# Optimization experiments

Measured on AMD Instinct MI355X. Metric: run time of the kernel, lower is better.

Reference implementation:

```python
import jax, jax.numpy as jnp
import numpy as np

B, S, E, C = 128, 512, 768, 9


def setup_inputs() -> dict:
    key = jax.random.key(0)
    ks = jax.random.split(key, 7)
    return {
        "enc": jax.random.normal(ks[0], (B, S, E), dtype=jnp.float32),
        "W": jax.random.normal(ks[1], (C, E), dtype=jnp.float32) * 0.02,
        "b": jax.random.normal(ks[2], (C,), dtype=jnp.float32) * 0.02,
        "start_transitions": jax.random.normal(ks[3], (C,), dtype=jnp.float32) * 0.1,
        "end_transitions": jax.random.normal(ks[4], (C,), dtype=jnp.float32) * 0.1,
        "transitions": jax.random.normal(ks[5], (C, C), dtype=jnp.float32) * 0.1,
        "tags": jax.random.randint(ks[6], (B, S), 0, C, dtype=jnp.int64),
        "mask": jnp.ones((B, S), dtype=bool),
    }


def _crf_nll_mean(emissions, tags, mask, start_transitions, end_transitions, transitions):
    # emissions: [B,S,C], tags: [B,S] int, mask: [B,S] bool (mask[:,0] all True)
    maskf = mask.astype(emissions.dtype)
    b_idx = jnp.arange(emissions.shape[0])
    # ---- numerator: score of the gold tag path ----
    em_tag = jnp.take_along_axis(emissions, tags[..., None], axis=2)[..., 0]  # [B,S]
    trans_pair = transitions[tags[:, :-1], tags[:, 1:]]  # [B,S-1]
    num = start_transitions[tags[:, 0]] + em_tag[:, 0]
    num = num + jnp.sum((trans_pair + em_tag[:, 1:]) * maskf[:, 1:], axis=1)
    seq_len = mask.sum(axis=1).astype(jnp.int32)
    last_tags = tags[b_idx, seq_len - 1]
    num = num + end_transitions[last_tags]
    # ---- denominator: forward algorithm (log partition) via scan ----
    def step(alpha, xs):
        em_t, m_t = xs  # [B,C], [B]
        # broadcast: alpha[b,i] + transitions[i,j] + em_t[b,j]
        nxt = jax.nn.logsumexp(alpha[:, :, None] + transitions[None, :, :] + em_t[:, None, :], axis=1)
        alpha = jnp.where(m_t[:, None], nxt, alpha)
        return alpha, None

    alpha0 = start_transitions[None, :] + emissions[:, 0]  # [B,C]
    em_rest = jnp.swapaxes(emissions[:, 1:], 0, 1)  # [S-1,B,C]
    m_rest = jnp.swapaxes(mask[:, 1:], 0, 1)        # [S-1,B]
    alpha, _ = jax.lax.scan(step, alpha0, (em_rest, m_rest))
    den = jax.nn.logsumexp(alpha + end_transitions[None, :], axis=1)  # [B]
    # reduction='mean' over batch; module returns -llh
    return jnp.mean(den - num)


def reference(enc, W, b, start_transitions, end_transitions, transitions, tags, mask):
    # BERT output `enc` is frozen (torch.no_grad); dropout omitted (deterministic ref)
    emissions = jnp.einsum("bse,ce->bsc", enc, W) + b  # linear head [B,S,C]
    return _crf_nll_mean(emissions, tags, mask, start_transitions, end_transitions, transitions)
```

## Files before the change

### kernel.cpp

```cpp
#include <hip/hip_runtime.h>

static constexpr int kB = 128;
static constexpr int kS = 512;
static constexpr int kE = 768;
static constexpr int kC = 9;
static constexpr int kT = 16;
static constexpr int kChunks = 32;

using bf16x8 = __attribute__((ext_vector_type(8))) short;
using f32x4  = __attribute__((ext_vector_type(4))) float;

__device__ __forceinline__ unsigned short f2bf(float f) {
  union { float f; unsigned u; } cv; cv.f = f;
  return (unsigned short)((cv.u + 0x7FFFu + ((cv.u >> 16) & 1u)) >> 16);
}

__global__ __launch_bounds__(256) void wconv_kernel(const float* __restrict__ W,
                                                    unsigned short* __restrict__ Wbf) {
  const int idx = blockIdx.x * 256 + threadIdx.x;
  if (idx < 16 * kE) Wbf[idx] = (idx < kC * kE) ? f2bf(W[idx]) : (unsigned short)0;
}

__global__ __launch_bounds__(128) void fused_chunk(
    const float* __restrict__ enc, const unsigned short* __restrict__ Wbf,
    const float* __restrict__ bias, const float* __restrict__ trans,
    const float* __restrict__ start_t, const float* __restrict__ end_t,
    const int* __restrict__ tags, float* __restrict__ Pout,
    float* __restrict__ numP) {
  __shared__ float emt[2 * kT * 12];
  __shared__ float P[81];
  __shared__ float atmp[16];
  __shared__ float nred[kT];

  const int blk = blockIdx.x;
  const int b = blk >> 5;
  const int k = blk & 31;
  const int tid = threadIdx.x;
  const int wv = tid >> 6;
  const int lane = tid & 63;
  const int mn = lane & 15;
  const int quad = lane >> 4;

  {
    const float* rp = enc + ((size_t)(b * kS + k * kT + mn)) * kE + wv * (kE / 2) + quad * 8;
    const unsigned short* wp = Wbf + mn * kE + wv * (kE / 2) + quad * 8;
    f32x4 acc = {0.f, 0.f, 0.f, 0.f};
#pragma unroll 4
    for (int s = 0; s < (kE / 2) / 32; ++s) {
      const float4 x0 = *reinterpret_cast<const float4*>(rp + s * 32);
      const float4 x1 = *reinterpret_cast<const float4*>(rp + s * 32 + 4);
      bf16x8 a;
      a[0] = (short)f2bf(x0.x); a[1] = (short)f2bf(x0.y);
      a[2] = (short)f2bf(x0.z); a[3] = (short)f2bf(x0.w);
      a[4] = (short)f2bf(x1.x); a[5] = (short)f2bf(x1.y);
      a[6] = (short)f2bf(x1.z); a[7] = (short)f2bf(x1.w);
      const bf16x8 bf = *reinterpret_cast<const bf16x8*>(wp + s * 32);
      acc = __builtin_amdgcn_mfma_f32_16x16x32_bf16(a, bf, acc, 0, 0, 0);
    }
    if (mn < kC) {
      const float bc = (wv == 0) ? bias[mn] : 0.f;
#pragma unroll
      for (int r = 0; r < 4; ++r)
        emt[wv * (kT * 12) + (quad * 4 + r) * 12 + mn] = acc[r] + bc;
    }
  }
  __syncthreads();

#define EM(t, c) (emt[(t) * 12 + (c)] + emt[kT * 12 + (t) * 12 + (c)])

  if (tid < kT) {
    const int t = k * kT + tid;
    const int ct = tags[b * kS + t];
    float v = EM(tid, ct);
    if (t == 0) v += start_t[ct];
    else        v += trans[tags[b * kS + t - 1] * kC + ct];
    if (t == kS - 1) v += end_t[ct];
    nred[tid] = v;
  }
  __syncthreads();
  if (tid == 0) {
    float s = 0.f;
#pragma unroll
    for (int i = 0; i < kT; ++i) s += nred[i];
    numP[blk] = s;
  }

  const bool act = tid < 81;
  const int ci = act ? (tid / 9) : 0;
  const int cj = act ? (tid - ci * 9) : 0;
  float tr[kC];
  if (act) {
#pragma unroll
    for (int kk = 0; kk < kC; ++kk) tr[kk] = trans[kk * kC + cj];
  }

  if (k == 0) {
    if (tid < kC) atmp[tid] = start_t[tid] + EM(0, tid);
    __syncthreads();
    for (int t = 1; t < kT; ++t) {
      float nv = 0.f;
      if (tid < kC) {
        float m = -3.0e38f, v[kC];
#pragma unroll
        for (int i = 0; i < kC; ++i) { v[i] = atmp[i] + tr[i]; m = fmaxf(m, v[i]); }
        float s = 0.f;
#pragma unroll
        for (int i = 0; i < kC; ++i) s += __expf(v[i] - m);
        nv = m + __logf(s) + EM(t, tid);
      }
      __syncthreads();
      if (tid < kC) atmp[tid] = nv;
      __syncthreads();
    }
    if (tid < kC) Pout[(size_t)blk * 81 + tid] = atmp[tid];
  } else {
    if (act) P[tid] = trans[ci * kC + cj] + EM(0, cj);
    __syncthreads();
    for (int t = 1; t < kT; ++t) {
      float nv = 0.f;
      if (act) {
        float m = -3.0e38f, v[kC];
#pragma unroll
        for (int kk = 0; kk < kC; ++kk) { v[kk] = P[ci * 9 + kk] + tr[kk]; m = fmaxf(m, v[kk]); }
        float s = 0.f;
#pragma unroll
        for (int kk = 0; kk < kC; ++kk) s += __expf(v[kk] - m);
        nv = m + __logf(s) + EM(t, cj);
      }
      __syncthreads();
      if (act) P[tid] = nv;
      __syncthreads();
    }
    if (act) Pout[(size_t)blk * 81 + cj * kC + ci] = P[tid];
  }
#undef EM
}

__global__ __launch_bounds__(64) void combine_kernel(const float* __restrict__ Pmat,
                                                     const float* __restrict__ numP,
                                                     const float* __restrict__ end_t,
                                                     float* __restrict__ out) {
  const int b = blockIdx.x;
  const int lane = threadIdx.x;

  float nsum = (lane < kChunks) ? numP[b * kChunks + lane] : 0.f;
#pragma unroll
  for (int m = 16; m >= 1; m >>= 1) nsum += __shfl_down(nsum, m, 64);

  const float* Pb = Pmat + (size_t)b * kChunks * 81;
  const int ln = (lane < kC) ? lane : 0;
  float alpha = Pb[ln];

  float p[kC];
#pragma unroll
  for (int i = 0; i < kC; ++i) p[i] = Pb[81 + ln * kC + i];

  for (int k = 1; k < kChunks; ++k) {
    float pn[kC];
    if (k + 1 < kChunks) {
      const float* Pn = Pb + (k + 1) * 81 + ln * kC;
#pragma unroll
      for (int i = 0; i < kC; ++i) pn[i] = Pn[i];
    }
    float tv[kC];
    float m = -3.0e38f;
#pragma unroll
    for (int i = 0; i < kC; ++i) {
      const float ai = __shfl(alpha, i, 64);
      tv[i] = ai + p[i];
      m = fmaxf(m, tv[i]);
    }
    float s = 0.f;
#pragma unroll
    for (int i = 0; i < kC; ++i) s += __expf(tv[i] - m);
    alpha = m + __logf(s);
#pragma unroll
    for (int i = 0; i < kC; ++i) p[i] = pn[i];
  }

  const float v = alpha + end_t[ln];
  float vv[kC];
  float m = -3.0e38f;
#pragma unroll
  for (int i = 0; i < kC; ++i) {
    vv[i] = __shfl(v, i, 64);
    m = fmaxf(m, vv[i]);
  }
  float s = 0.f;
#pragma unroll
  for (int i = 0; i < kC; ++i) s += __expf(vv[i] - m);
  if (lane == 0) {
    const float den = m + __logf(s);
    atomicAdd(out, (den - nsum) * (1.0f / (float)kB));
  }
}

extern "C" void kernel_launch(void* const* d_in, const int* in_sizes, int n_in,
                              void* d_out, int out_size, void* d_ws, size_t ws_size,
                              hipStream_t stream) {
  const float* enc   = (const float*)d_in[0];
  const float* W     = (const float*)d_in[1];
  const float* bias  = (const float*)d_in[2];
  const float* start = (const float*)d_in[3];
  const float* end_t = (const float*)d_in[4];
  const float* trans = (const float*)d_in[5];
  const int*   tags  = (const int*)d_in[6];

  unsigned short* Wbf = (unsigned short*)d_ws;
  float* Pmat = (float*)((char*)d_ws + 16 * kE * sizeof(unsigned short));
  float* numP = Pmat + (size_t)kB * kChunks * 81;
  float* out  = (float*)d_out;

  hipMemsetAsync(out, 0, sizeof(float), stream);
  hipLaunchKernelGGL(wconv_kernel, dim3((16 * kE + 255) / 256), dim3(256), 0, stream, W, Wbf);
  hipLaunchKernelGGL(fused_chunk, dim3(kB * kChunks), dim3(128), 0, stream,
                     enc, Wbf, bias, trans, start, end_t, tags, Pmat, numP);
  hipLaunchKernelGGL(combine_kernel, dim3(kB), dim3(64), 0, stream, Pmat, numP, end_t, out);
}
```

Baseline: 308.0 us.

## Run chunk scan in one wavefront with wave barriers and packed bf16 conversion

The per-chunk forward scan is moved from a two-wave block using __syncthreads to a single wavefront. Each lane handles up to two of the 81 matrix entries, with wave barriers and float4 LDS reads. The second wave now only computes the gold-path numerator with shuffles and exits early. The emission partial sums are merged into one LDS buffer, and fp32→bf16 conversion uses the packed HIP intrinsic. The aim is to cut block-wide barrier cost and conversion instructions, at the cost of a more serial per-lane workload in the scan.

```diff
diff --git a/kernel.cpp b/kernel.cpp
--- a/kernel.cpp
+++ b/kernel.cpp
@@ -1,4 +1,5 @@
 #include <hip/hip_runtime.h>
+#include <hip/hip_bf16.h>
 
 static constexpr int kB = 128;
 static constexpr int kS = 512;
@@ -15,6 +16,13 @@
   return (unsigned short)((cv.u + 0x7FFFu + ((cv.u >> 16) & 1u)) >> 16);
 }
 
+__device__ __forceinline__ short2 cvt2(float lo, float hi) {
+  const __hip_bfloat162 h = __float22bfloat162_rn(make_float2(lo, hi));
+  short2 r;
+  __builtin_memcpy(&r, &h, sizeof(r));
+  return r;
+}
+
 __global__ __launch_bounds__(256) void wconv_kernel(const float* __restrict__ W,
                                                     unsigned short* __restrict__ Wbf) {
   const int idx = blockIdx.x * 256 + threadIdx.x;
@@ -27,10 +35,8 @@
     const float* __restrict__ start_t, const float* __restrict__ end_t,
     const int* __restrict__ tags, float* __restrict__ Pout,
     float* __restrict__ numP) {
-  __shared__ float emt[2 * kT * 12];
-  __shared__ float P[81];
-  __shared__ float atmp[16];
-  __shared__ float nred[kT];
+  __shared__ __align__(16) float emt[kT * 12];
+  __shared__ __align__(16) float P[kC * 12];
 
   const int blk = blockIdx.x;
   const int b = blk >> 5;
@@ -41,99 +47,129 @@
   const int mn = lane & 15;
   const int quad = lane >> 4;
 
+  f32x4 acc = {0.f, 0.f, 0.f, 0.f};
   {
     const float* rp = enc + ((size_t)(b * kS + k * kT + mn)) * kE + wv * (kE / 2) + quad * 8;
     const unsigned short* wp = Wbf + mn * kE + wv * (kE / 2) + quad * 8;
-    f32x4 acc = {0.f, 0.f, 0.f, 0.f};
 #pragma unroll 4
     for (int s = 0; s < (kE / 2) / 32; ++s) {
       const float4 x0 = *reinterpret_cast<const float4*>(rp + s * 32);
       const float4 x1 = *reinterpret_cast<const float4*>(rp + s * 32 + 4);
+      const short2 p0 = cvt2(x0.x, x0.y);
+      const short2 p1 = cvt2(x0.z, x0.w);
+      const short2 p2 = cvt2(x1.x, x1.y);
+      const short2 p3 = cvt2(x1.z, x1.w);
       bf16x8 a;
-      a[0] = (short)f2bf(x0.x); a[1] = (short)f2bf(x0.y);
-      a[2] = (short)f2bf(x0.z); a[3] = (short)f2bf(x0.w);
-      a[4] = (short)f2bf(x1.x); a[5] = (short)f2bf(x1.y);
-      a[6] = (short)f2bf(x1.z); a[7] = (short)f2bf(x1.w);
+      a[0] = p0.x; a[1] = p0.y; a[2] = p1.x; a[3] = p1.y;
+      a[4] = p2.x; a[5] = p2.y; a[6] = p3.x; a[7] = p3.y;
       const bf16x8 bf = *reinterpret_cast<const bf16x8*>(wp + s * 32);
       acc = __builtin_amdgcn_mfma_f32_16x16x32_bf16(a, bf, acc, 0, 0, 0);
     }
-    if (mn < kC) {
-      const float bc = (wv == 0) ? bias[mn] : 0.f;
-#pragma unroll
-      for (int r = 0; r < 4; ++r)
-        emt[wv * (kT * 12) + (quad * 4 + r) * 12 + mn] = acc[r] + bc;
-    }
+  }
+  if (wv == 0 && mn < kC) {
+    const float bc = bias[mn];
+#pragma unroll
+    for (int r = 0; r < 4; ++r) emt[(quad * 4 + r) * 12 + mn] = acc[r] + bc;
   }
   __syncthreads();
-
-#define EM(t, c) (emt[(t) * 12 + (c)] + emt[kT * 12 + (t) * 12 + (c)])
-
-  if (tid < kT) {
-    const int t = k * kT + tid;
-    const int ct = tags[b * kS + t];
-    float v = EM(tid, ct);
-    if (t == 0) v += start_t[ct];
-    else        v += trans[tags[b * kS + t - 1] * kC + ct];
-    if (t == kS - 1) v += end_t[ct];
-    nred[tid] = v;
+  if (wv == 1 && mn < kC) {
+#pragma unroll
+    for (int r = 0; r < 4; ++r) emt[(quad * 4 + r) * 12 + mn] += acc[r];
   }
   __syncthreads();
-  if (tid == 0) {
-    float s = 0.f;
-#pragma unroll
-    for (int i = 0; i < kT; ++i) s += nred[i];
-    numP[blk] = s;
-  }
-
-  const bool act = tid < 81;
-  const int ci = act ? (tid / 9) : 0;
-  const int cj = act ? (tid - ci * 9) : 0;
-  float tr[kC];
-  if (act) {
-#pragma unroll
-    for (int kk = 0; kk < kC; ++kk) tr[kk] = trans[kk * kC + cj];
+
+  if (wv == 1) {
+    float v = 0.f;
+    if (lane < kT) {
+      const int t = k * kT + lane;
+      const int ct = tags[b * kS + t];
+      v = emt[lane * 12 + ct];
+      if (t == 0) v += start_t[ct];
+      else        v += trans[tags[b * kS + t - 1] * kC + ct];
+      if (t == kS - 1) v += end_t[ct];
+    }
+    v += __shfl_down(v, 8, 64);
+    v += __shfl_down(v, 4, 64);
+    v += __shfl_down(v, 2, 64);
+    v += __shfl_down(v, 1, 64);
+    if (lane == 0) numP[blk] = v;
+    return;
   }
 
   if (k == 0) {
-    if (tid < kC) atmp[tid] = start_t[tid] + EM(0, tid);
-    __syncthreads();
+    if (lane < kC) {
+      float tr[kC];
+#pragma unroll
+      for (int i = 0; i < kC; ++i) tr[i] = trans[i * kC + lane];
+      float alpha = start_t[lane] + emt[lane];
+      for (int t = 1; t < kT; ++t) {
+        float m = -3.0e38f, v[kC];
+#pragma unroll
+        for (int i = 0; i < kC; ++i) { v[i] = __shfl(alpha, i, 64) + tr[i]; m = fmaxf(m, v[i]); }
+        float s = 0.f;
+#pragma unroll
+        for (int i = 0; i < kC; ++i) s += __expf(v[i] - m);
+        alpha = m + __logf(s) + emt[t * 12 + lane];
+      }
+      Pout[(size_t)blk * 81 + lane] = alpha;
+    }
+  } else {
+    const int ci0 = lane / 9, cj0 = lane - ci0 * 9;
+    const bool has1 = (lane < 17);
+    const int e1 = 64 + lane;
+    const int ci1 = e1 / 9, cj1 = e1 - (e1 / 9) * 9;
+
+    float tr0[kC], tr1[kC];
+#pragma unroll
+    for (int kk = 0; kk < kC; ++kk) tr0[kk] = trans[kk * kC + cj0];
+    if (has1) {
+#pragma unroll
+      for (int kk = 0; kk < kC; ++kk) tr1[kk] = trans[kk * kC + cj1];
+    }
+
+    float cur0 = trans[ci0 * kC + cj0] + emt[cj0];
+    float cur1 = 0.f;
+    P[ci0 * 12 + cj0] = cur0;
+    if (has1) { cur1 = trans[ci1 * kC + cj1] + emt[cj1]; P[ci1 * 12 + cj1] = cur1; }
+
     for (int t = 1; t < kT; ++t) {
-      float nv = 0.f;
-      if (tid < kC) {
-        float m = -3.0e38f, v[kC];
-#pragma unroll
-        for (int i = 0; i < kC; ++i) { v[i] = atmp[i] + tr[i]; m = fmaxf(m, v[i]); }
+      __builtin_amdgcn_wave_barrier();
+      const float4 a0 = *reinterpret_cast<const float4*>(&P[ci0 * 12]);
+      const float4 a4 = *reinterpret_cast<const float4*>(&P[ci0 * 12 + 4]);
+      const float a8 = P[ci0 * 12 + 8];
+      float4 b0, b4; float b8 = 0.f;
+      if (has1) {
+        b0 = *reinterpret_cast<const float4*>(&P[ci1 * 12]);
+        b4 = *reinterpret_cast<const float4*>(&P[ci1 * 12 + 4]);
+        b8 = P[ci1 * 12 + 8];
+      }
+      {
+        float pr[kC] = {a0.x, a0.y, a0.z, a0.w, a4.x, a4.y, a4.z, a4.w, a8};
+        float m = -3.0e38f, tv[kC];
+#pragma unroll
+        for (int kk = 0; kk < kC; ++kk) { tv[kk] = pr[kk] + tr0[kk]; m = fmaxf(m, tv[kk]); }
         float s = 0.f;
 #pragma unroll
-        for (int i = 0; i < kC; ++i) s += __expf(v[i] - m);
-        nv = m + __logf(s) + EM(t, tid);
-      }
-      __syncthreads();
-      if (tid < kC) atmp[tid] = nv;
-      __syncthreads();
-    }
-    if (tid < kC) Pout[(size_t)blk * 81 + tid] = atmp[tid];
-  } else {
-    if (act) P[tid] = trans[ci * kC + cj] + EM(0, cj);
-    __syncthreads();
-    for (int t = 1; t < kT; ++t) {
-      float nv = 0.f;
-      if (act) {
-        float m = -3.0e38f, v[kC];
-#pragma unroll
-        for (int kk = 0; kk < kC; ++kk) { v[kk] = P[ci * 9 + kk] + tr[kk]; m = fmaxf(m, v[kk]); }
+        for (int kk = 0; kk < kC; ++kk) s += __expf(tv[kk] - m);
+        cur0 = m + __logf(s) + emt[t * 12 + cj0];
+      }
+      if (has1) {
+        float pr[kC] = {b0.x, b0.y, b0.z, b0.w, b4.x, b4.y, b4.z, b4.w, b8};
+        float m = -3.0e38f, tv[kC];
+#pragma unroll
+        for (int kk = 0; kk < kC; ++kk) { tv[kk] = pr[kk] + tr1[kk]; m = fmaxf(m, tv[kk]); }
         float s = 0.f;
 #pragma unroll
-        for (int kk = 0; kk < kC; ++kk) s += __expf(v[kk] - m);
-        nv = m + __logf(s) + EM(t, cj);
-      }
-      __syncthreads();
-      if (act) P[tid] = nv;
-      __syncthreads();
-    }
-    if (act) Pout[(size_t)blk * 81 + cj * kC + ci] = P[tid];
-  }
-#undef EM
+        for (int kk = 0; kk < kC; ++kk) s += __expf(tv[kk] - m);
+        cur1 = m + __logf(s) + emt[t * 12 + cj1];
+      }
+      __builtin_amdgcn_wave_barrier();
+      P[ci0 * 12 + cj0] = cur0;
+      if (has1) P[ci1 * 12 + cj1] = cur1;
+    }
+    Pout[(size_t)blk * 81 + cj0 * kC + ci0] = cur0;
+    if (has1) Pout[(size_t)blk * 81 + cj1 * kC + ci1] = cur1;
+  }
 }
 
 __global__ __launch_bounds__(64) void combine_kernel(const float* __restrict__ Pmat,
@@ -211,7 +247,7 @@
   float* numP = Pmat + (size_t)kB * kChunks * 81;
   float* out  = (float*)d_out;
 
-  hipMemsetAsync(out, 0, sizeof(float), stream);
+  (void)hipMemsetAsync(out, 0, sizeof(float), stream);
   hipLaunchKernelGGL(wconv_kernel, dim3((16 * kE + 255) / 256), dim3(256), 0, stream, W, Wbf);
   hipLaunchKernelGGL(fused_chunk, dim3(kB * kChunks), dim3(128), 0, stream,
                      enc, Wbf, bias, trans, start, end_t, tags, Pmat, numP);
```

Result: slower. 322.4 us (+4.7%).

## Fuse chunk combine into main kernel via last-block atomic counter

Applied to the files above, without the earlier changes.

Removes the separate combine kernel and the memset. A per-batch atomic counter lets the last chunk block of each batch run the sequential log-semiring combine, and the counter and output are now zeroed inside the weight-conversion kernel. This saves two launches and their gaps, at the cost of threadfences and an atomic in every block, plus a serial tail that runs in whichever block finishes last.

```diff
diff --git a/kernel.cpp b/kernel.cpp
--- a/kernel.cpp
+++ b/kernel.cpp
@@ -16,9 +16,15 @@
 }
 
 __global__ __launch_bounds__(256) void wconv_kernel(const float* __restrict__ W,
-                                                    unsigned short* __restrict__ Wbf) {
+                                                    unsigned short* __restrict__ Wbf,
+                                                    unsigned* __restrict__ cnt,
+                                                    float* __restrict__ out) {
   const int idx = blockIdx.x * 256 + threadIdx.x;
   if (idx < 16 * kE) Wbf[idx] = (idx < kC * kE) ? f2bf(W[idx]) : (unsigned short)0;
+  if (blockIdx.x == 0) {
+    if (threadIdx.x < kB) cnt[threadIdx.x] = 0u;
+    else if (threadIdx.x == kB) *out = 0.f;
+  }
 }
 
 __global__ __launch_bounds__(128) void fused_chunk(
@@ -26,7 +32,8 @@
     const float* __restrict__ bias, const float* __restrict__ trans,
     const float* __restrict__ start_t, const float* __restrict__ end_t,
     const int* __restrict__ tags, float* __restrict__ Pout,
-    float* __restrict__ numP) {
+    float* __restrict__ numP, unsigned* __restrict__ cnt,
+    float* __restrict__ out) {
   __shared__ float emt[2 * kT * 12];
   __shared__ float P[81];
   __shared__ float atmp[16];
@@ -134,64 +141,67 @@
     if (act) Pout[(size_t)blk * 81 + cj * kC + ci] = P[tid];
   }
 #undef EM
-}
-
-__global__ __launch_bounds__(64) void combine_kernel(const float* __restrict__ Pmat,
-                                                     const float* __restrict__ numP,
-                                                     const float* __restrict__ end_t,
-                                                     float* __restrict__ out) {
-  const int b = blockIdx.x;
-  const int lane = threadIdx.x;
-
-  float nsum = (lane < kChunks) ? numP[b * kChunks + lane] : 0.f;
-#pragma unroll
-  for (int m = 16; m >= 1; m >>= 1) nsum += __shfl_down(nsum, m, 64);
-
-  const float* Pb = Pmat + (size_t)b * kChunks * 81;
-  const int ln = (lane < kC) ? lane : 0;
-  float alpha = Pb[ln];
-
-  float p[kC];
-#pragma unroll
-  for (int i = 0; i < kC; ++i) p[i] = Pb[81 + ln * kC + i];
-
-  for (int k = 1; k < kChunks; ++k) {
-    float pn[kC];
-    if (k + 1 < kChunks) {
-      const float* Pn = Pb + (k + 1) * 81 + ln * kC;
-#pragma unroll
-      for (int i = 0; i < kC; ++i) pn[i] = Pn[i];
-    }
-    float tv[kC];
-    float m = -3.0e38f;
-#pragma unroll
-    for (int i = 0; i < kC; ++i) {
-      const float ai = __shfl(alpha, i, 64);
-      tv[i] = ai + p[i];
-      m = fmaxf(m, tv[i]);
-    }
-    float s = 0.f;
-#pragma unroll
-    for (int i = 0; i < kC; ++i) s += __expf(tv[i] - m);
-    alpha = m + __logf(s);
-#pragma unroll
-    for (int i = 0; i < kC; ++i) p[i] = pn[i];
-  }
-
-  const float v = alpha + end_t[ln];
-  float vv[kC];
-  float m = -3.0e38f;
-#pragma unroll
-  for (int i = 0; i < kC; ++i) {
-    vv[i] = __shfl(v, i, 64);
-    m = fmaxf(m, vv[i]);
-  }
-  float s = 0.f;
-#pragma unroll
-  for (int i = 0; i < kC; ++i) s += __expf(vv[i] - m);
-  if (lane == 0) {
-    const float den = m + __logf(s);
-    atomicAdd(out, (den - nsum) * (1.0f / (float)kB));
+
+  __syncthreads();
+  if (tid < 64) {
+    __threadfence();
+    unsigned old_c = 0;
+    if (tid == 0) old_c = atomicAdd(&cnt[b], 1u);
+    old_c = __shfl(old_c, 0, 64);
+    if (old_c == kChunks - 1) {
+      __threadfence();
+
+      float nsum = (lane < kChunks) ? numP[b * kChunks + lane] : 0.f;
+#pragma unroll
+      for (int m = 16; m >= 1; m >>= 1) nsum += __shfl_down(nsum, m, 64);
+
+      const float* Pb = Pout + (size_t)b * kChunks * 81;
+      const int ln = (lane < kC) ? lane : 0;
+      float alpha = Pb[ln];
+
+      float p[kC];
+#pragma unroll
+      for (int i = 0; i < kC; ++i) p[i] = Pb[81 + ln * kC + i];
+
+      for (int kk = 1; kk < kChunks; ++kk) {
+        float pn[kC];
+        if (kk + 1 < kChunks) {
+          const float* Pn = Pb + (kk + 1) * 81 + ln * kC;
+#pragma unroll
+          for (int i = 0; i < kC; ++i) pn[i] = Pn[i];
+        }
+        float tv[kC];
+        float m = -3.0e38f;
+#pragma unroll
+        for (int i = 0; i < kC; ++i) {
+          const float ai = __shfl(alpha, i, 64);
+          tv[i] = ai + p[i];
+          m = fmaxf(m, tv[i]);
+        }
+        float s = 0.f;
+#pragma unroll
+        for (int i = 0; i < kC; ++i) s += __expf(tv[i] - m);
+        alpha = m + __logf(s);
+#pragma unroll
+        for (int i = 0; i < kC; ++i) p[i] = pn[i];
+      }
+
+      const float v = alpha + end_t[ln];
+      float vv[kC];
+      float m = -3.0e38f;
+#pragma unroll
+      for (int i = 0; i < kC; ++i) {
+        vv[i] = __shfl(v, i, 64);
+        m = fmaxf(m, vv[i]);
+      }
+      float s = 0.f;
+#pragma unroll
+      for (int i = 0; i < kC; ++i) s += __expf(vv[i] - m);
+      if (lane == 0) {
+        const float den = m + __logf(s);
+        atomicAdd(out, (den - nsum) * (1.0f / (float)kB));
+      }
+    }
   }
 }
 
@@ -209,11 +219,11 @@
   unsigned short* Wbf = (unsigned short*)d_ws;
   float* Pmat = (float*)((char*)d_ws + 16 * kE * sizeof(unsigned short));
   float* numP = Pmat + (size_t)kB * kChunks * 81;
+  unsigned* cnt = (unsigned*)(numP + kB * kChunks);
   float* out  = (float*)d_out;
 
-  hipMemsetAsync(out, 0, sizeof(float), stream);
-  hipLaunchKernelGGL(wconv_kernel, dim3((16 * kE + 255) / 256), dim3(256), 0, stream, W, Wbf);
+  hipLaunchKernelGGL(wconv_kernel, dim3((16 * kE + 255) / 256), dim3(256), 0, stream,
+                     W, Wbf, cnt, out);
   hipLaunchKernelGGL(fused_chunk, dim3(kB * kChunks), dim3(128), 0, stream,
-                     enc, Wbf, bias, trans, start, end_t, tags, Pmat, numP);
-  hipLaunchKernelGGL(combine_kernel, dim3(kB), dim3(64), 0, stream, Pmat, numP, end_t, out);
-}
+                     enc, Wbf, bias, trans, start, end_t, tags, Pmat, numP, cnt, out);
+}
```

Result: slower. 499.5 us (+62.2%).

## Run chunk forward recursion in linear probability space with matrix products

Applied to the files above, without the earlier changes.

Rewrites the per-chunk CRF forward scan so it works on exponentiated transitions and emissions. Each step becomes a 9-term dot product instead of a logsumexp, with a constant offset subtracted to keep values in range. This removes the per-step max/exp/log work and merges the k==0 and k>0 paths. The two-wave emission reduction moves into shared memory, the numerator sum uses wave shuffles, and the ping-pong buffer needs one barrier per step instead of two. The trade-off is a risk of overflow or underflow in linear space over 16 steps.

```diff
diff --git a/kernel.cpp b/kernel.cpp
--- a/kernel.cpp
+++ b/kernel.cpp
@@ -27,10 +27,8 @@
     const float* __restrict__ start_t, const float* __restrict__ end_t,
     const int* __restrict__ tags, float* __restrict__ Pout,
     float* __restrict__ numP) {
-  __shared__ float emt[2 * kT * 12];
-  __shared__ float P[81];
-  __shared__ float atmp[16];
-  __shared__ float nred[kT];
+  __shared__ __align__(16) float emt[kT * 12];
+  __shared__ __align__(16) float Plin[2][kC * 12];
 
   const int blk = blockIdx.x;
   const int b = blk >> 5;
@@ -57,83 +55,88 @@
       const bf16x8 bf = *reinterpret_cast<const bf16x8*>(wp + s * 32);
       acc = __builtin_amdgcn_mfma_f32_16x16x32_bf16(a, bf, acc, 0, 0, 0);
     }
-    if (mn < kC) {
-      const float bc = (wv == 0) ? bias[mn] : 0.f;
-#pragma unroll
-      for (int r = 0; r < 4; ++r)
-        emt[wv * (kT * 12) + (quad * 4 + r) * 12 + mn] = acc[r] + bc;
-    }
-  }
-  __syncthreads();
-
-#define EM(t, c) (emt[(t) * 12 + (c)] + emt[kT * 12 + (t) * 12 + (c)])
-
-  if (tid < kT) {
-    const int t = k * kT + tid;
-    const int ct = tags[b * kS + t];
-    float v = EM(tid, ct);
-    if (t == 0) v += start_t[ct];
-    else        v += trans[tags[b * kS + t - 1] * kC + ct];
-    if (t == kS - 1) v += end_t[ct];
-    nred[tid] = v;
-  }
-  __syncthreads();
-  if (tid == 0) {
-    float s = 0.f;
-#pragma unroll
-    for (int i = 0; i < kT; ++i) s += nred[i];
-    numP[blk] = s;
+    if (wv == 0 && mn < kC) {
+      const float bc = bias[mn];
+#pragma unroll
+      for (int r = 0; r < 4; ++r) emt[(quad * 4 + r) * 12 + mn] = acc[r] + bc;
+    }
+    __syncthreads();
+    if (wv == 1 && mn < kC) {
+#pragma unroll
+      for (int r = 0; r < 4; ++r) emt[(quad * 4 + r) * 12 + mn] += acc[r];
+    }
+    __syncthreads();
+  }
+
+  if (wv == 0) {
+    float v = 0.f;
+    if (lane < kT) {
+      const int t = k * kT + lane;
+      const int ct = tags[b * kS + t];
+      v = emt[lane * 12 + ct];
+      if (t == 0) v += start_t[ct];
+      else        v += trans[tags[b * kS + t - 1] * kC + ct];
+      if (t == kS - 1) v += end_t[ct];
+    }
+    v += __shfl_down(v, 8, 64);
+    v += __shfl_down(v, 4, 64);
+    v += __shfl_down(v, 2, 64);
+    v += __shfl_down(v, 1, 64);
+    if (lane == 0) numP[blk] = v;
   }
 
   const bool act = tid < 81;
   const int ci = act ? (tid / 9) : 0;
   const int cj = act ? (tid - ci * 9) : 0;
-  float tr[kC];
+
+  float Ecol[kC];
+  float cur = 0.f;
   if (act) {
 #pragma unroll
-    for (int kk = 0; kk < kC; ++kk) tr[kk] = trans[kk * kC + cj];
-  }
-
-  if (k == 0) {
-    if (tid < kC) atmp[tid] = start_t[tid] + EM(0, tid);
-    __syncthreads();
-    for (int t = 1; t < kT; ++t) {
-      float nv = 0.f;
-      if (tid < kC) {
-        float m = -3.0e38f, v[kC];
-#pragma unroll
-        for (int i = 0; i < kC; ++i) { v[i] = atmp[i] + tr[i]; m = fmaxf(m, v[i]); }
-        float s = 0.f;
-#pragma unroll
-        for (int i = 0; i < kC; ++i) s += __expf(v[i] - m);
-        nv = m + __logf(s) + EM(t, tid);
-      }
+    for (int kk = 0; kk < kC; ++kk) Ecol[kk] = __expf(trans[kk * kC + cj] - 1.0f);
+    const float g0 = __expf(emt[cj]);
+    const float base = (k == 0) ? __expf(start_t[cj] - 1.0f) : Ecol[ci];
+    cur = base * g0;
+    Plin[0][ci * 12 + cj] = cur;
+  }
+  __syncthreads();
+
+  int pb = 0;
+  for (int t = 1; t < kT; ++t) {
+    float nv = 0.f;
+    if (act) {
+      const float* Pr = &Plin[pb][ci * 12];
+      const float4 a0 = *reinterpret_cast<const float4*>(Pr);
+      const float4 a4 = *reinterpret_cast<const float4*>(Pr + 4);
+      const float a8 = Pr[8];
+      float s;
+      s  = a0.x * Ecol[0];
+      s += a0.y * Ecol[1];
+      s += a0.z * Ecol[2];
+      s += a0.w * Ecol[3];
+      s += a4.x * Ecol[4];
+      s += a4.y * Ecol[5];
+      s += a4.z * Ecol[6];
+      s += a4.w * Ecol[7];
+      s += a8   * Ecol[8];
+      nv = s * __expf(emt[t * 12 + cj]);
+    }
+    if (t < kT - 1) {
+      if (act) Plin[pb ^ 1][ci * 12 + cj] = nv;
       __syncthreads();
-      if (tid < kC) atmp[tid] = nv;
-      __syncthreads();
-    }
-    if (tid < kC) Pout[(size_t)blk * 81 + tid] = atmp[tid];
-  } else {
-    if (act) P[tid] = trans[ci * kC + cj] + EM(0, cj);
-    __syncthreads();
-    for (int t = 1; t < kT; ++t) {
-      float nv = 0.f;
-      if (act) {
-        float m = -3.0e38f, v[kC];
-#pragma unroll
-        for (int kk = 0; kk < kC; ++kk) { v[kk] = P[ci * 9 + kk] + tr[kk]; m = fmaxf(m, v[kk]); }
-        float s = 0.f;
-#pragma unroll
-        for (int kk = 0; kk < kC; ++kk) s += __expf(v[kk] - m);
-        nv = m + __logf(s) + EM(t, cj);
-      }
-      __syncthreads();
-      if (act) P[tid] = nv;
-      __syncthreads();
-    }
-    if (act) Pout[(size_t)blk * 81 + cj * kC + ci] = P[tid];
-  }
-#undef EM
+      pb ^= 1;
+    }
+    cur = nv;
+  }
+
+  if (act) {
+    const float res = __logf(cur) + (float)kT;
+    if (k == 0) {
+      if (ci == 0) Pout[(size_t)blk * 81 + cj] = res;
+    } else {
+      Pout[(size_t)blk * 81 + cj * kC + ci] = res;
+    }
+  }
 }
 
 __global__ __launch_bounds__(64) void combine_kernel(const float* __restrict__ Pmat,
@@ -211,7 +214,7 @@
   float* numP = Pmat + (size_t)kB * kChunks * 81;
   float* out  = (float*)d_out;
 
-  hipMemsetAsync(out, 0, sizeof(float), stream);
+  (void)hipMemsetAsync(out, 0, sizeof(float), stream);
   hipLaunchKernelGGL(wconv_kernel, dim3((16 * kE + 255) / 256), dim3(256), 0, stream, W, Wbf);
   hipLaunchKernelGGL(fused_chunk, dim3(kB * kChunks), dim3(128), 0, stream,
                      enc, Wbf, bias, trans, start, end_t, tags, Pmat, numP);
```

Measured after the change: 304.8 us. About the same (-1.1%).
